# Performance work log

Measured on AMD Instinct MI355X. Metric: run time of the kernel, lower is better.

## Reference

```python
import jax, jax.numpy as jnp
import numpy as np
from jax import lax

V, D = 100000, 300          # vocab, embedding dim (pretrained_embeds shape)
F, FS, K = 256, 3, 5        # nof_filters, filters_size, k_for_maxpool
B, NS, LS, LQ = 64, 50, 60, 32  # batch, n_sents per doc, sent len, question len


def setup_inputs() -> dict:
    key = jax.random.key(0)
    ks = jax.random.split(key, 8)
    sentences = jax.random.randint(ks[0], (B, NS, LS), 0, V)
    question = jax.random.randint(ks[1], (B, LQ), 0, V)
    target_sents = jax.random.randint(ks[2], (B, NS), 0, 2)
    target_docs = jax.random.randint(ks[3], (B,), 0, 2)
    embeds = jax.random.normal(ks[4], (V, D), dtype=jnp.float32)          # frozen pretrained table
    filters = jax.random.normal(ks[5], (F, 1, FS, D), dtype=jnp.float32)  # shared quest/sent conv filters
    W = jax.random.normal(ks[6], (6,), dtype=jnp.float32) * 0.4           # linear_per_q weight
    b = jax.random.normal(ks[7], (1,), dtype=jnp.float32) * 0.1           # linear_per_q bias
    return dict(sentences=sentences, question=question, target_sents=target_sents,
                target_docs=target_docs, embeds=embeds, filters=filters, W=W, b=b)


def _conv(x, filters):
    # x: [N,L,D], filters: [F,1,FS,D] -> [N,L,F]; matches F.conv2d(pad=(FS-1,0)) then slicing last L rows
    fs = filters.shape[2]
    L = x.shape[1]
    y = lax.conv_general_dilated(x[:, None, :, :], filters, (1, 1),
                                 ((fs - 1, fs - 1), (0, 0)),
                                 dimension_numbers=('NCHW', 'OIHW', 'NCHW'))  # [N,F,L+fs-1,1]
    return jnp.transpose(y[:, :, -L:, 0], (0, 2, 1))


def _cos(q, s):
    # q: [B,LQ,d], s: [B,NS,LS,d] -> [NS,B,LQ,LS] cosine similarity matrices
    num = jnp.einsum('bqd,bnld->nbql', q, s)
    qn = jnp.linalg.norm(q, axis=-1)                      # [B,LQ]
    sn = jnp.transpose(jnp.linalg.norm(s, axis=-1), (1, 0, 2))  # [NS,B,LS]
    return num / (qn[None, :, :, None] * sn[:, :, None, :])


def _pool(sim, k):
    # k-max pooling over the sentence-length axis -> stack [max, mean-of-top-k]
    top = lax.top_k(sim, k)[0]
    return jnp.stack([top[..., 0], jnp.mean(top, axis=-1)], axis=-1)


def _bce(p, t):
    eps = 1e-7
    p = jnp.clip(p, eps, 1.0 - eps)
    return -jnp.mean(t * jnp.log(p) + (1.0 - t) * jnp.log1p(-p))


def reference(sentences, question, target_sents, target_docs, embeds, filters, W, b):
    qe = embeds[question]                                 # [B,LQ,D]
    se = embeds[sentences]                                # [B,NS,LS,D]
    sim_ins = _cos(qe, se)                                # [NS,B,LQ,LS]
    sim_oh = (sim_ins >= 1.0 - 1e-5).astype(jnp.float32)  # exact-match channel (unmasked, as in original)
    qc = _conv(qe, filters)                               # [B,LQ,F]
    sc = _conv(se.reshape(B * NS, LS, D), filters).reshape(B, NS, LS, F)
    sim_sen = _cos(qc, sc)                                # [NS,B,LQ,LS]
    qmask = (question > 0).astype(jnp.float32)            # pad id = 0
    smask = (sentences > 0).astype(jnp.float32)
    m = qmask[None, :, :, None] * jnp.transpose(smask, (1, 0, 2))[:, :, None, :]
    feats = jnp.concatenate([_pool(sim_ins * m, K), _pool(sim_sen * m, K), _pool(sim_oh, K)], axis=-1)
    feats = jnp.transpose(feats, (1, 0, 2, 3))            # [B,NS,LQ,6]
    sent_out = jax.nn.sigmoid(feats @ W + b[0])           # [B,NS,LQ]
    sentence_relevance = jnp.mean(sent_out, axis=-1)      # [B,NS]
    document_emitions = jnp.max(sentence_relevance, axis=-1)  # [B]
    loss = (_bce(sentence_relevance, target_sents.astype(jnp.float32)) +
            _bce(document_emitions, target_docs.astype(jnp.float32))) / 2.0
    return loss, sentence_relevance, document_emitions
```

## Files before the change

kernel.cpp:

```cpp
#include <hip/hip_runtime.h>
#include <math.h>

#define VB  64
#define NSS 50
#define LSS 60
#define LQQ 32
#define DD  300
#define FF  256

#define SEST 312
#define SROWS 66
#define SCST 264
#define SIMST 66
#define KKC 29
#define KKI 10
#define KKS 8

typedef __attribute__((ext_vector_type(8))) short bfrag;
typedef __attribute__((ext_vector_type(4))) float ffrag;

__device__ __forceinline__ unsigned short f2bf(float v) {
    unsigned int x = __float_as_uint(v);
    x += 0x7fffu + ((x >> 16) & 1u);
    return (unsigned short)(x >> 16);
}
__device__ __forceinline__ float bf2f(unsigned short u) {
    return __uint_as_float(((unsigned int)u) << 16);
}

__global__ __launch_bounds__(256) void k_fprep(const float* __restrict__ filters,
                                               unsigned short* __restrict__ filt_frag) {
    int idx = blockIdx.x * 256 + threadIdx.x;
    const int total = KKC * 16 * 64 * 8;
    if (idx >= total) return;
    int j = idx & 7, ln = (idx >> 3) & 63, nt = (idx >> 9) & 15, kk = idx >> 13;
    int f = nt * 16 + (ln & 15);
    int k = kk * 32 + ((ln >> 4) << 3) + j;
    int t = k / SEST, d = k - t * SEST;
    unsigned short v = 0;
    if (t < 3 && d < DD) v = f2bf(filters[f * 900 + t * DD + d]);
    filt_frag[idx] = v;
}

__global__ __launch_bounds__(256) void k_qprep(const int* __restrict__ question,
                                               const float* __restrict__ embeds,
                                               const unsigned short* __restrict__ filt_frag,
                                               unsigned short* __restrict__ qe_frag,
                                               unsigned short* __restrict__ qc_frag,
                                               float* __restrict__ q_inv,
                                               float* __restrict__ qc_inv) {
    const int b = blockIdx.x, tid = threadIdx.x, lane = tid & 63, w = tid >> 6;
    const int quad = lane >> 4, m16 = lane & 15;
    __shared__ __align__(16) unsigned short qeb[34 * SEST];
    __shared__ __align__(16) unsigned short qcb[LQQ * SCST];
    __shared__ int qid[LQQ];
    if (tid < LQQ) qid[tid] = question[b * LQQ + tid];
    {
        ushort4 z4 = {0, 0, 0, 0};
        for (int i = tid; i < 96; i += 256) {
            int r = i / 3, c = 300 + (i - r * 3) * 4;
            *(ushort4*)(qeb + r * SEST + c) = z4;
        }
        for (int i = tid; i < 156; i += 256) {
            int r = i / 78, c = (i - r * 78) * 4;
            *(ushort4*)(qeb + (LQQ + r) * SEST + c) = z4;
        }
    }
    __syncthreads();
    for (int i = tid; i < LQQ * 75; i += 256) {
        int r = i / 75, c = (i - r * 75) * 4;
        float4 v = *(const float4*)(embeds + (size_t)qid[r] * DD + c);
        ushort4 h;
        h.x = f2bf(v.x); h.y = f2bf(v.y); h.z = f2bf(v.z); h.w = f2bf(v.w);
        *(ushort4*)(qeb + r * SEST + c) = h;
    }
    __syncthreads();
    {
        int r = tid >> 3, part = tid & 7;
        float s = 0.f;
        for (int c = part * 4; c < DD; c += 32) {
            uint2 u = *(const uint2*)(qeb + r * SEST + c);
            float a0 = bf2f((unsigned short)(u.x & 0xffff)), a1 = bf2f((unsigned short)(u.x >> 16));
            float a2 = bf2f((unsigned short)(u.y & 0xffff)), a3 = bf2f((unsigned short)(u.y >> 16));
            s += a0 * a0 + a1 * a1 + a2 * a2 + a3 * a3;
        }
        s += __shfl_down(s, 4, 64);
        s += __shfl_down(s, 2, 64);
        s += __shfl_down(s, 1, 64);
        if (part == 0) q_inv[b * LQQ + r] = 1.f / sqrtf(s);
    }
    for (int idx = tid; idx < KKI * 2 * 512; idx += 256) {
        int j = idx & 7, ln = (idx >> 3) & 63, mt = (idx >> 9) & 1, kk = idx >> 10;
        int q = mt * 16 + (ln & 15);
        int k = kk * 32 + ((ln >> 4) << 3) + j;
        qe_frag[(size_t)b * (KKI * 2 * 512) + idx] = (k < DD) ? qeb[q * SEST + k] : (unsigned short)0;
    }
    ffrag acc[2][4];
    #pragma unroll
    for (int mt = 0; mt < 2; ++mt)
        #pragma unroll
        for (int i = 0; i < 4; ++i) acc[mt][i] = (ffrag)0.f;
    {
        const bfrag* fF = (const bfrag*)filt_frag;
        const int w4 = w * 4;
        for (int kk = 0; kk < KKC; ++kk) {
            const int kb = kk * 32 + quad * 8;
            bfrag a0 = *(const bfrag*)(qeb + m16 * SEST + kb);
            bfrag a1 = *(const bfrag*)(qeb + (16 + m16) * SEST + kb);
            bfrag bb[4];
            #pragma unroll
            for (int i = 0; i < 4; ++i) bb[i] = fF[(kk * 16 + w4 + i) * 64 + lane];
            #pragma unroll
            for (int i = 0; i < 4; ++i) {
                acc[0][i] = __builtin_amdgcn_mfma_f32_16x16x32_bf16(a0, bb[i], acc[0][i], 0, 0, 0);
                acc[1][i] = __builtin_amdgcn_mfma_f32_16x16x32_bf16(a1, bb[i], acc[1][i], 0, 0, 0);
            }
        }
    }
    #pragma unroll
    for (int mt = 0; mt < 2; ++mt)
        #pragma unroll
        for (int i = 0; i < 4; ++i) {
            int f = (w * 4 + i) * 16 + m16;
            #pragma unroll
            for (int r = 0; r < 4; ++r) {
                int q = mt * 16 + quad * 4 + r;
                qcb[q * SCST + f] = f2bf(acc[mt][i][r]);
            }
        }
    __syncthreads();
    {
        int r = tid >> 3, part = tid & 7;
        float s = 0.f;
        for (int c = part * 4; c < FF; c += 32) {
            uint2 u = *(const uint2*)(qcb + r * SCST + c);
            float a0 = bf2f((unsigned short)(u.x & 0xffff)), a1 = bf2f((unsigned short)(u.x >> 16));
            float a2 = bf2f((unsigned short)(u.y & 0xffff)), a3 = bf2f((unsigned short)(u.y >> 16));
            s += a0 * a0 + a1 * a1 + a2 * a2 + a3 * a3;
        }
        s += __shfl_down(s, 4, 64);
        s += __shfl_down(s, 2, 64);
        s += __shfl_down(s, 1, 64);
        if (part == 0) qc_inv[b * LQQ + r] = 1.f / sqrtf(s);
    }
    for (int idx = tid; idx < KKS * 2 * 512; idx += 256) {
        int j = idx & 7, ln = (idx >> 3) & 63, mt = (idx >> 9) & 1, kk = idx >> 10;
        int q = mt * 16 + (ln & 15);
        int k = kk * 32 + ((ln >> 4) << 3) + j;
        qc_frag[(size_t)b * (KKS * 2 * 512) + idx] = qcb[q * SCST + k];
    }
}

__global__ __launch_bounds__(512, 6) void k_sent(
    const int* __restrict__ sentences, const int* __restrict__ question,
    const float* __restrict__ embeds,
    const unsigned short* __restrict__ filt_frag,
    const unsigned short* __restrict__ qe_frag,
    const unsigned short* __restrict__ qc_frag,
    const float* __restrict__ q_inv, const float* __restrict__ qc_inv,
    const float* __restrict__ W6, const float* __restrict__ b1,
    float* __restrict__ d_out) {
    const int blk = blockIdx.x;
    const int b = blk / NSS, n = blk - b * NSS;
    const int tid = threadIdx.x, lane = tid & 63, w = tid >> 6;
    const int quad = lane >> 4, m16 = lane & 15;

    __shared__ __align__(16) unsigned short seb[SROWS * SEST];
    __shared__ __align__(16) float sim[LQQ * SIMST];
    __shared__ float sinv[64], scninv[64];
    __shared__ int sid[64];
    __shared__ int qid[LQQ];
    __shared__ float qm[LQQ], qiv[LQQ], qciv[LQQ];
    __shared__ float featq[LQQ][4];
    __shared__ float pr[LQQ];
    unsigned short* scb = seb;

    if (tid < 64) sid[tid] = (tid < LSS) ? sentences[((size_t)b * NSS + n) * LSS + tid] : 0;
    if (tid < LQQ) {
        int qi = question[b * LQQ + tid];
        qid[tid] = qi; qm[tid] = qi > 0 ? 1.f : 0.f;
        qiv[tid] = q_inv[b * LQQ + tid]; qciv[tid] = qc_inv[b * LQQ + tid];
    }
    {
        ushort4 z4 = {0, 0, 0, 0};
        for (int i = tid; i < 180; i += 512) {
            int r = i / 3, c = 300 + (i - r * 3) * 4;
            *(ushort4*)(seb + r * SEST + c) = z4;
        }
        for (int i = tid; i < 468; i += 512) {
            int r = i / 78, c = (i - r * 78) * 4;
            *(ushort4*)(seb + (60 + r) * SEST + c) = z4;
        }
    }
    __syncthreads();
    for (int i = tid; i < LSS * 75; i += 512) {
        int r = i / 75, c = (i - r * 75) * 4;
        float4 v = *(const float4*)(embeds + (size_t)sid[r] * DD + c);
        ushort4 h;
        h.x = f2bf(v.x); h.y = f2bf(v.y); h.z = f2bf(v.z); h.w = f2bf(v.w);
        *(ushort4*)(seb + r * SEST + c) = h;
    }
    __syncthreads();
    if (tid < 480) {
        int r = tid >> 3, part = tid & 7;
        float s = 0.f;
        for (int c = part * 4; c < DD; c += 32) {
            uint2 u = *(const uint2*)(seb + r * SEST + c);
            float a0 = bf2f((unsigned short)(u.x & 0xffff)), a1 = bf2f((unsigned short)(u.x >> 16));
            float a2 = bf2f((unsigned short)(u.y & 0xffff)), a3 = bf2f((unsigned short)(u.y >> 16));
            s += a0 * a0 + a1 * a1 + a2 * a2 + a3 * a3;
        }
        s += __shfl_down(s, 4, 64);
        s += __shfl_down(s, 2, 64);
        s += __shfl_down(s, 1, 64);
        if (part == 0) sinv[r] = 1.f / sqrtf(s);
    }
    if (tid >= 480 && tid < 484) sinv[60 + tid - 480] = 0.f;
    __syncthreads();

    ffrag acc[4][2];
    #pragma unroll
    for (int mt = 0; mt < 4; ++mt)
        #pragma unroll
        for (int i = 0; i < 2; ++i) acc[mt][i] = (ffrag)0.f;
    {
        const bfrag* fF = (const bfrag*)filt_frag;
        const int w2 = w * 2;
        for (int kk = 0; kk < KKC; ++kk) {
            const int kb = kk * 32 + quad * 8;
            bfrag a[4];
            #pragma unroll
            for (int mt = 0; mt < 4; ++mt)
                a[mt] = *(const bfrag*)(seb + (mt * 16 + m16) * SEST + kb);
            bfrag bb[2];
            #pragma unroll
            for (int i = 0; i < 2; ++i)
                bb[i] = fF[(kk * 16 + w2 + i) * 64 + lane];
            #pragma unroll
            for (int mt = 0; mt < 4; ++mt)
                #pragma unroll
                for (int i = 0; i < 2; ++i)
                    acc[mt][i] = __builtin_amdgcn_mfma_f32_16x16x32_bf16(a[mt], bb[i], acc[mt][i], 0, 0, 0);
        }
    }
    {
        const bfrag* qF = (const bfrag*)qe_frag;
        const int mt = w >> 2, nt = w & 3;
        ffrag c0 = (ffrag)0.f;
        for (int kk = 0; kk < KKI; ++kk) {
            bfrag aq = qF[((size_t)(b * KKI + kk) * 2 + mt) * 64 + lane];
            bfrag b0 = *(const bfrag*)(seb + (nt * 16 + m16) * SEST + kk * 32 + quad * 8);
            c0 = __builtin_amdgcn_mfma_f32_16x16x32_bf16(aq, b0, c0, 0, 0, 0);
        }
        const int l_ = nt * 16 + m16;
        const float sm = sinv[l_] * (sid[l_] > 0 ? 1.f : 0.f);
        #pragma unroll
        for (int r = 0; r < 4; ++r) {
            int q = mt * 16 + quad * 4 + r;
            sim[q * SIMST + l_] = c0[r] * (qiv[q] * qm[q]) * sm;
        }
    }
    __syncthreads();

    if (tid < 256) {
        ushort4 z4 = {0, 0, 0, 0};
        int r4 = 60 + (tid >> 6), c4 = (tid & 63) * 4;
        *(ushort4*)(scb + r4 * SCST + c4) = z4;
    }
    #pragma unroll
    for (int mt = 0; mt < 4; ++mt)
        #pragma unroll
        for (int i = 0; i < 2; ++i) {
            int f = (w * 2 + i) * 16 + m16;
            #pragma unroll
            for (int r = 0; r < 4; ++r) {
                int l = mt * 16 + quad * 4 + r;
                scb[l * SCST + f] = f2bf(acc[mt][i][r]);
            }
        }
    if (tid < LQQ) {
        int q = tid;
        float t0 = -1e30f, t1 = -1e30f, t2 = -1e30f, t3 = -1e30f, t4 = -1e30f;
        for (int l = 0; l < LSS; ++l) {
            float v = sim[q * SIMST + l];
            if (v > t4) {
                if (v > t0)      { t4 = t3; t3 = t2; t2 = t1; t1 = t0; t0 = v; }
                else if (v > t1) { t4 = t3; t3 = t2; t2 = t1; t1 = v; }
                else if (v > t2) { t4 = t3; t3 = t2; t2 = v; }
                else if (v > t3) { t4 = t3; t3 = v; }
                else               t4 = v;
            }
        }
        featq[q][0] = t0;
        featq[q][1] = (t0 + t1 + t2 + t3 + t4) * 0.2f;
        int qi = qid[q], c = 0;
        for (int l = 0; l < LSS; ++l) c += (sid[l] == qi) ? 1 : 0;
        featq[q][2] = c > 0 ? 1.f : 0.f;
        featq[q][3] = (float)(c < 5 ? c : 5) * 0.2f;
    }
    __syncthreads();
    if (tid < 480) {
        int r = tid >> 3, part = tid & 7;
        float s = 0.f;
        for (int c = part * 4; c < FF; c += 32) {
            uint2 u = *(const uint2*)(scb + r * SCST + c);
            float a0 = bf2f((unsigned short)(u.x & 0xffff)), a1 = bf2f((unsigned short)(u.x >> 16));
            float a2 = bf2f((unsigned short)(u.y & 0xffff)), a3 = bf2f((unsigned short)(u.y >> 16));
            s += a0 * a0 + a1 * a1 + a2 * a2 + a3 * a3;
        }
        s += __shfl_down(s, 4, 64);
        s += __shfl_down(s, 2, 64);
        s += __shfl_down(s, 1, 64);
        if (part == 0) scninv[r] = 1.f / sqrtf(s);
    }
    if (tid >= 480 && tid < 484) scninv[60 + tid - 480] = 0.f;
    __syncthreads();
    {
        const bfrag* qF = (const bfrag*)qc_frag;
        const int mt = w >> 2, nt = w & 3;
        ffrag c0 = (ffrag)0.f;
        for (int kk = 0; kk < KKS; ++kk) {
            bfrag aq = qF[((size_t)(b * KKS + kk) * 2 + mt) * 64 + lane];
            bfrag b0 = *(const bfrag*)(scb + (nt * 16 + m16) * SCST + kk * 32 + quad * 8);
            c0 = __builtin_amdgcn_mfma_f32_16x16x32_bf16(aq, b0, c0, 0, 0, 0);
        }
        const int l_ = nt * 16 + m16;
        const float sm = scninv[l_] * (sid[l_] > 0 ? 1.f : 0.f);
        #pragma unroll
        for (int r = 0; r < 4; ++r) {
            int q = mt * 16 + quad * 4 + r;
            sim[q * SIMST + l_] = c0[r] * (qciv[q] * qm[q]) * sm;
        }
    }
    __syncthreads();
    if (tid < LQQ) {
        int q = tid;
        float t0 = -1e30f, t1 = -1e30f, t2 = -1e30f, t3 = -1e30f, t4 = -1e30f;
        for (int l = 0; l < LSS; ++l) {
            float v = sim[q * SIMST + l];
            if (v > t4) {
                if (v > t0)      { t4 = t3; t3 = t2; t2 = t1; t1 = t0; t0 = v; }
                else if (v > t1) { t4 = t3; t3 = t2; t2 = t1; t1 = v; }
                else if (v > t2) { t4 = t3; t3 = t2; t2 = v; }
                else if (v > t3) { t4 = t3; t3 = v; }
                else               t4 = v;
            }
        }
        float smax = t0, smean = (t0 + t1 + t2 + t3 + t4) * 0.2f;
        float z = featq[q][0] * W6[0] + featq[q][1] * W6[1] + smax * W6[2] + smean * W6[3]
                + featq[q][2] * W6[4] + featq[q][3] * W6[5] + b1[0];
        pr[q] = 1.f / (1.f + expf(-z));
    }
    __syncthreads();
    if (w == 0) {
        float s = (lane < LQQ) ? pr[lane] : 0.f;
        s += __shfl_down(s, 16, 64);
        s += __shfl_down(s, 8, 64);
        s += __shfl_down(s, 4, 64);
        s += __shfl_down(s, 2, 64);
        s += __shfl_down(s, 1, 64);
        if (lane == 0) d_out[1 + (size_t)b * NSS + n] = s * (1.f / 32.f);
    }
}

__global__ __launch_bounds__(256) void k_final(const int* __restrict__ tsent,
                                               const int* __restrict__ tdoc,
                                               float* __restrict__ d_out) {
    const int tid = threadIdx.x;
    __shared__ float sh[256];
    __shared__ float docs[VB];
    if (tid < VB) {
        float m = -1e30f;
        for (int nn = 0; nn < NSS; ++nn) m = fmaxf(m, d_out[1 + tid * NSS + nn]);
        docs[tid] = m;
        d_out[1 + VB * NSS + tid] = m;
    }
    float s = 0.f;
    for (int i = tid; i < VB * NSS; i += 256) {
        float p = d_out[1 + i];
        p = fminf(fmaxf(p, 1e-7f), 1.f - 1e-7f);
        float t = (float)tsent[i];
        s += t * logf(p) + (1.f - t) * log1pf(-p);
    }
    sh[tid] = s;
    __syncthreads();
    for (int st = 128; st > 0; st >>= 1) {
        if (tid < st) sh[tid] += sh[tid + st];
        __syncthreads();
    }
    float ls = 0.f;
    if (tid == 0) ls = -sh[0] / (float)(VB * NSS);
    __syncthreads();
    float s2 = 0.f;
    if (tid < VB) {
        float p = fminf(fmaxf(docs[tid], 1e-7f), 1.f - 1e-7f);
        float t = (float)tdoc[tid];
        s2 = t * logf(p) + (1.f - t) * log1pf(-p);
    }
    sh[tid] = s2;
    __syncthreads();
    for (int st = 128; st > 0; st >>= 1) {
        if (tid < st) sh[tid] += sh[tid + st];
        __syncthreads();
    }
    if (tid == 0) {
        float ld = -sh[0] / (float)VB;
        d_out[0] = 0.5f * (ls + ld);
    }
}

extern "C" void kernel_launch(void* const* d_in, const int* in_sizes, int n_in,
                              void* d_out, int out_size, void* d_ws, size_t ws_size,
                              hipStream_t stream) {
    const int*   sentences = (const int*)d_in[0];
    const int*   question  = (const int*)d_in[1];
    const int*   tsent     = (const int*)d_in[2];
    const int*   tdoc      = (const int*)d_in[3];
    const float* embeds    = (const float*)d_in[4];
    const float* filters   = (const float*)d_in[5];
    const float* W6        = (const float*)d_in[6];
    const float* b1        = (const float*)d_in[7];
    float* out = (float*)d_out;

    float* ws = (float*)d_ws;
    float* q_inv  = ws;
    float* qc_inv = ws + 2048;
    unsigned short* qe_frag  = (unsigned short*)(ws + 4096);
    unsigned short* qc_frag  = qe_frag + 655360;
    unsigned short* filt_frag = qc_frag + 524288;

    k_fprep<<<928, 256, 0, stream>>>(filters, filt_frag);
    k_qprep<<<VB, 256, 0, stream>>>(question, embeds, filt_frag, qe_frag, qc_frag, q_inv, qc_inv);
    k_sent<<<VB * NSS, 512, 0, stream>>>(sentences, question, embeds,
                                         filt_frag, qe_frag, qc_frag,
                                         q_inv, qc_inv, W6, b1, out);
    k_final<<<1, 256, 0, stream>>>(tsent, tdoc, out);
}
```

Measured before the change: 411.0 us.

## Software-pipeline filter fragment loads in conv and widen norm reads

The sentence conv loop is unrolled by two and double-buffers the global filter fragments, with the first fragments issued before the embedding gather, and MFMA groups wrapped in s_setprio. The cosine GEMM loops prefetch the next question fragment, and the norm reductions read 16-byte LDS vectors. One barrier is removed by reading token ids straight from global memory, and the question prep kernel moves to 512 threads with work split across 8 waves. The aim is to hide global-load latency behind MFMA work and cut LDS instruction count, at the cost of more live registers under the 512x6 launch bound.

Measured after the change: 401.8 us. 2.2% less time.

```diff
diff --git a/kernel.cpp b/kernel.cpp
--- a/kernel.cpp
+++ b/kernel.cpp
@@ -42,7 +42,7 @@
     filt_frag[idx] = v;
 }
 
-__global__ __launch_bounds__(256) void k_qprep(const int* __restrict__ question,
+__global__ __launch_bounds__(512) void k_qprep(const int* __restrict__ question,
                                                const float* __restrict__ embeds,
                                                const unsigned short* __restrict__ filt_frag,
                                                unsigned short* __restrict__ qe_frag,
@@ -53,103 +53,122 @@
     const int quad = lane >> 4, m16 = lane & 15;
     __shared__ __align__(16) unsigned short qeb[34 * SEST];
     __shared__ __align__(16) unsigned short qcb[LQQ * SCST];
-    __shared__ int qid[LQQ];
-    if (tid < LQQ) qid[tid] = question[b * LQQ + tid];
+    const int* qrow = question + b * LQQ;
     {
         ushort4 z4 = {0, 0, 0, 0};
-        for (int i = tid; i < 96; i += 256) {
+        for (int i = tid; i < 96; i += 512) {
             int r = i / 3, c = 300 + (i - r * 3) * 4;
             *(ushort4*)(qeb + r * SEST + c) = z4;
         }
-        for (int i = tid; i < 156; i += 256) {
+        for (int i = tid; i < 156; i += 512) {
             int r = i / 78, c = (i - r * 78) * 4;
             *(ushort4*)(qeb + (LQQ + r) * SEST + c) = z4;
         }
     }
-    __syncthreads();
-    for (int i = tid; i < LQQ * 75; i += 256) {
+    for (int i = tid; i < LQQ * 75; i += 512) {
         int r = i / 75, c = (i - r * 75) * 4;
-        float4 v = *(const float4*)(embeds + (size_t)qid[r] * DD + c);
+        float4 v = *(const float4*)(embeds + (size_t)qrow[r] * DD + c);
         ushort4 h;
         h.x = f2bf(v.x); h.y = f2bf(v.y); h.z = f2bf(v.z); h.w = f2bf(v.w);
         *(ushort4*)(qeb + r * SEST + c) = h;
     }
     __syncthreads();
-    {
+    if (tid < 256) {
         int r = tid >> 3, part = tid & 7;
         float s = 0.f;
-        for (int c = part * 4; c < DD; c += 32) {
-            uint2 u = *(const uint2*)(qeb + r * SEST + c);
-            float a0 = bf2f((unsigned short)(u.x & 0xffff)), a1 = bf2f((unsigned short)(u.x >> 16));
-            float a2 = bf2f((unsigned short)(u.y & 0xffff)), a3 = bf2f((unsigned short)(u.y >> 16));
-            s += a0 * a0 + a1 * a1 + a2 * a2 + a3 * a3;
+        #pragma unroll
+        for (int it = 0; it < 5; ++it) {
+            if (!(it == 4 && part == 7)) {
+                int c = part * 8 + it * 64;
+                uint4 u = *(const uint4*)(qeb + r * SEST + c);
+                float a0 = bf2f((unsigned short)(u.x & 0xffff)), a1 = bf2f((unsigned short)(u.x >> 16));
+                float a2 = bf2f((unsigned short)(u.y & 0xffff)), a3 = bf2f((unsigned short)(u.y >> 16));
+                float a4 = bf2f((unsigned short)(u.z & 0xffff)), a5 = bf2f((unsigned short)(u.z >> 16));
+                float a6 = bf2f((unsigned short)(u.w & 0xffff)), a7 = bf2f((unsigned short)(u.w >> 16));
+                s += a0 * a0 + a1 * a1 + a2 * a2 + a3 * a3 + a4 * a4 + a5 * a5 + a6 * a6 + a7 * a7;
+            }
         }
         s += __shfl_down(s, 4, 64);
         s += __shfl_down(s, 2, 64);
         s += __shfl_down(s, 1, 64);
         if (part == 0) q_inv[b * LQQ + r] = 1.f / sqrtf(s);
     }
-    for (int idx = tid; idx < KKI * 2 * 512; idx += 256) {
+    for (int idx = tid; idx < KKI * 2 * 512; idx += 512) {
         int j = idx & 7, ln = (idx >> 3) & 63, mt = (idx >> 9) & 1, kk = idx >> 10;
         int q = mt * 16 + (ln & 15);
         int k = kk * 32 + ((ln >> 4) << 3) + j;
         qe_frag[(size_t)b * (KKI * 2 * 512) + idx] = (k < DD) ? qeb[q * SEST + k] : (unsigned short)0;
     }
-    ffrag acc[2][4];
+    const int mtq = w & 1, w4 = (w >> 1) * 4;
+    ffrag acc[4];
     #pragma unroll
-    for (int mt = 0; mt < 2; ++mt)
-        #pragma unroll
-        for (int i = 0; i < 4; ++i) acc[mt][i] = (ffrag)0.f;
+    for (int i = 0; i < 4; ++i) acc[i] = (ffrag)0.f;
     {
         const bfrag* fF = (const bfrag*)filt_frag;
-        const int w4 = w * 4;
         for (int kk = 0; kk < KKC; ++kk) {
             const int kb = kk * 32 + quad * 8;
-            bfrag a0 = *(const bfrag*)(qeb + m16 * SEST + kb);
-            bfrag a1 = *(const bfrag*)(qeb + (16 + m16) * SEST + kb);
+            bfrag a0 = *(const bfrag*)(qeb + (mtq * 16 + m16) * SEST + kb);
             bfrag bb[4];
             #pragma unroll
             for (int i = 0; i < 4; ++i) bb[i] = fF[(kk * 16 + w4 + i) * 64 + lane];
             #pragma unroll
-            for (int i = 0; i < 4; ++i) {
-                acc[0][i] = __builtin_amdgcn_mfma_f32_16x16x32_bf16(a0, bb[i], acc[0][i], 0, 0, 0);
-                acc[1][i] = __builtin_amdgcn_mfma_f32_16x16x32_bf16(a1, bb[i], acc[1][i], 0, 0, 0);
-            }
+            for (int i = 0; i < 4; ++i)
+                acc[i] = __builtin_amdgcn_mfma_f32_16x16x32_bf16(a0, bb[i], acc[i], 0, 0, 0);
         }
     }
     #pragma unroll
-    for (int mt = 0; mt < 2; ++mt)
-        #pragma unroll
-        for (int i = 0; i < 4; ++i) {
-            int f = (w * 4 + i) * 16 + m16;
-            #pragma unroll
-            for (int r = 0; r < 4; ++r) {
-                int q = mt * 16 + quad * 4 + r;
-                qcb[q * SCST + f] = f2bf(acc[mt][i][r]);
-            }
-        }
-    __syncthreads();
-    {
+    for (int i = 0; i < 4; ++i) {
+        int f = (w4 + i) * 16 + m16;
+        #pragma unroll
+        for (int r = 0; r < 4; ++r) {
+            int q = mtq * 16 + quad * 4 + r;
+            qcb[q * SCST + f] = f2bf(acc[i][r]);
+        }
+    }
+    __syncthreads();
+    if (tid < 256) {
         int r = tid >> 3, part = tid & 7;
         float s = 0.f;
-        for (int c = part * 4; c < FF; c += 32) {
-            uint2 u = *(const uint2*)(qcb + r * SCST + c);
+        #pragma unroll
+        for (int it = 0; it < 4; ++it) {
+            int c = part * 8 + it * 64;
+            uint4 u = *(const uint4*)(qcb + r * SCST + c);
             float a0 = bf2f((unsigned short)(u.x & 0xffff)), a1 = bf2f((unsigned short)(u.x >> 16));
             float a2 = bf2f((unsigned short)(u.y & 0xffff)), a3 = bf2f((unsigned short)(u.y >> 16));
-            s += a0 * a0 + a1 * a1 + a2 * a2 + a3 * a3;
+            float a4 = bf2f((unsigned short)(u.z & 0xffff)), a5 = bf2f((unsigned short)(u.z >> 16));
+            float a6 = bf2f((unsigned short)(u.w & 0xffff)), a7 = bf2f((unsigned short)(u.w >> 16));
+            s += a0 * a0 + a1 * a1 + a2 * a2 + a3 * a3 + a4 * a4 + a5 * a5 + a6 * a6 + a7 * a7;
         }
         s += __shfl_down(s, 4, 64);
         s += __shfl_down(s, 2, 64);
         s += __shfl_down(s, 1, 64);
         if (part == 0) qc_inv[b * LQQ + r] = 1.f / sqrtf(s);
     }
-    for (int idx = tid; idx < KKS * 2 * 512; idx += 256) {
+    for (int idx = tid; idx < KKS * 2 * 512; idx += 512) {
         int j = idx & 7, ln = (idx >> 3) & 63, mt = (idx >> 9) & 1, kk = idx >> 10;
         int q = mt * 16 + (ln & 15);
         int k = kk * 32 + ((ln >> 4) << 3) + j;
         qc_frag[(size_t)b * (KKS * 2 * 512) + idx] = qcb[q * SCST + k];
     }
 }
+
+#define CONV_STEP(KKV, BB0, BB1) do {                                              \
+    const int kb_ = (KKV) * 32 + quad * 8;                                         \
+    bfrag a0_ = *(const bfrag*)(seb + (m16) * SEST + kb_);                         \
+    bfrag a1_ = *(const bfrag*)(seb + (16 + m16) * SEST + kb_);                    \
+    bfrag a2_ = *(const bfrag*)(seb + (32 + m16) * SEST + kb_);                    \
+    bfrag a3_ = *(const bfrag*)(seb + (48 + m16) * SEST + kb_);                    \
+    __builtin_amdgcn_s_setprio(1);                                                 \
+    acc[0][0] = __builtin_amdgcn_mfma_f32_16x16x32_bf16(a0_, BB0, acc[0][0], 0, 0, 0); \
+    acc[0][1] = __builtin_amdgcn_mfma_f32_16x16x32_bf16(a0_, BB1, acc[0][1], 0, 0, 0); \
+    acc[1][0] = __builtin_amdgcn_mfma_f32_16x16x32_bf16(a1_, BB0, acc[1][0], 0, 0, 0); \
+    acc[1][1] = __builtin_amdgcn_mfma_f32_16x16x32_bf16(a1_, BB1, acc[1][1], 0, 0, 0); \
+    acc[2][0] = __builtin_amdgcn_mfma_f32_16x16x32_bf16(a2_, BB0, acc[2][0], 0, 0, 0); \
+    acc[2][1] = __builtin_amdgcn_mfma_f32_16x16x32_bf16(a2_, BB1, acc[2][1], 0, 0, 0); \
+    acc[3][0] = __builtin_amdgcn_mfma_f32_16x16x32_bf16(a3_, BB0, acc[3][0], 0, 0, 0); \
+    acc[3][1] = __builtin_amdgcn_mfma_f32_16x16x32_bf16(a3_, BB1, acc[3][1], 0, 0, 0); \
+    __builtin_amdgcn_s_setprio(0);                                                 \
+} while (0)
 
 __global__ __launch_bounds__(512, 6) void k_sent(
     const int* __restrict__ sentences, const int* __restrict__ question,
@@ -164,6 +183,7 @@
     const int b = blk / NSS, n = blk - b * NSS;
     const int tid = threadIdx.x, lane = tid & 63, w = tid >> 6;
     const int quad = lane >> 4, m16 = lane & 15;
+    const int w2 = w * 2;
 
     __shared__ __align__(16) unsigned short seb[SROWS * SEST];
     __shared__ __align__(16) float sim[LQQ * SIMST];
@@ -175,7 +195,12 @@
     __shared__ float pr[LQQ];
     unsigned short* scb = seb;
 
-    if (tid < 64) sid[tid] = (tid < LSS) ? sentences[((size_t)b * NSS + n) * LSS + tid] : 0;
+    const bfrag* fF = (const bfrag*)filt_frag;
+    bfrag b0a = fF[(w2) * 64 + lane];
+    bfrag b0b = fF[(w2 + 1) * 64 + lane];
+
+    const int* srow = sentences + ((size_t)b * NSS + n) * LSS;
+    if (tid < 64) sid[tid] = (tid < LSS) ? srow[tid] : 0;
     if (tid < LQQ) {
         int qi = question[b * LQQ + tid];
         qid[tid] = qi; qm[tid] = qi > 0 ? 1.f : 0.f;
@@ -192,10 +217,9 @@
             *(ushort4*)(seb + (60 + r) * SEST + c) = z4;
         }
     }
-    __syncthreads();
     for (int i = tid; i < LSS * 75; i += 512) {
         int r = i / 75, c = (i - r * 75) * 4;
-        float4 v = *(const float4*)(embeds + (size_t)sid[r] * DD + c);
+        float4 v = *(const float4*)(embeds + (size_t)srow[r] * DD + c);
         ushort4 h;
         h.x = f2bf(v.x); h.y = f2bf(v.y); h.z = f2bf(v.z); h.w = f2bf(v.w);
         *(ushort4*)(seb + r * SEST + c) = h;
@@ -204,11 +228,17 @@
     if (tid < 480) {
         int r = tid >> 3, part = tid & 7;
         float s = 0.f;
-        for (int c = part * 4; c < DD; c += 32) {
-            uint2 u = *(const uint2*)(seb + r * SEST + c);
-            float a0 = bf2f((unsigned short)(u.x & 0xffff)), a1 = bf2f((unsigned short)(u.x >> 16));
-            float a2 = bf2f((unsigned short)(u.y & 0xffff)), a3 = bf2f((unsigned short)(u.y >> 16));
-            s += a0 * a0 + a1 * a1 + a2 * a2 + a3 * a3;
+        #pragma unroll
+        for (int it = 0; it < 5; ++it) {
+            if (!(it == 4 && part == 7)) {
+                int c = part * 8 + it * 64;
+                uint4 u = *(const uint4*)(seb + r * SEST + c);
+                float a0 = bf2f((unsigned short)(u.x & 0xffff)), a1 = bf2f((unsigned short)(u.x >> 16));
+                float a2 = bf2f((unsigned short)(u.y & 0xffff)), a3 = bf2f((unsigned short)(u.y >> 16));
+                float a4 = bf2f((unsigned short)(u.z & 0xffff)), a5 = bf2f((unsigned short)(u.z >> 16));
+                float a6 = bf2f((unsigned short)(u.w & 0xffff)), a7 = bf2f((unsigned short)(u.w >> 16));
+                s += a0 * a0 + a1 * a1 + a2 * a2 + a3 * a3 + a4 * a4 + a5 * a5 + a6 * a6 + a7 * a7;
+            }
         }
         s += __shfl_down(s, 4, 64);
         s += __shfl_down(s, 2, 64);
@@ -224,33 +254,32 @@
         #pragma unroll
         for (int i = 0; i < 2; ++i) acc[mt][i] = (ffrag)0.f;
     {
-        const bfrag* fF = (const bfrag*)filt_frag;
-        const int w2 = w * 2;
-        for (int kk = 0; kk < KKC; ++kk) {
-            const int kb = kk * 32 + quad * 8;
-            bfrag a[4];
-            #pragma unroll
-            for (int mt = 0; mt < 4; ++mt)
-                a[mt] = *(const bfrag*)(seb + (mt * 16 + m16) * SEST + kb);
-            bfrag bb[2];
-            #pragma unroll
-            for (int i = 0; i < 2; ++i)
-                bb[i] = fF[(kk * 16 + w2 + i) * 64 + lane];
-            #pragma unroll
-            for (int mt = 0; mt < 4; ++mt)
-                #pragma unroll
-                for (int i = 0; i < 2; ++i)
-                    acc[mt][i] = __builtin_amdgcn_mfma_f32_16x16x32_bf16(a[mt], bb[i], acc[mt][i], 0, 0, 0);
-        }
-    }
-    {
-        const bfrag* qF = (const bfrag*)qe_frag;
+        bfrag b1a, b1b;
+        for (int kk = 0; kk + 2 <= KKC; kk += 2) {
+            b1a = fF[((kk + 1) * 16 + w2) * 64 + lane];
+            b1b = fF[((kk + 1) * 16 + w2 + 1) * 64 + lane];
+            CONV_STEP(kk, b0a, b0b);
+            if (kk + 2 < KKC) {
+                b0a = fF[((kk + 2) * 16 + w2) * 64 + lane];
+                b0b = fF[((kk + 2) * 16 + w2 + 1) * 64 + lane];
+            }
+            CONV_STEP(kk + 1, b1a, b1b);
+        }
+        CONV_STEP(KKC - 1, b0a, b0b);
+    }
+    {
         const int mt = w >> 2, nt = w & 3;
+        const bfrag* qF = (const bfrag*)qe_frag + ((size_t)b * KKI * 2 + mt) * 64 + lane;
+        const unsigned short* sebr = seb + (nt * 16 + m16) * SEST + quad * 8;
         ffrag c0 = (ffrag)0.f;
-        for (int kk = 0; kk < KKI; ++kk) {
-            bfrag aq = qF[((size_t)(b * KKI + kk) * 2 + mt) * 64 + lane];
-            bfrag b0 = *(const bfrag*)(seb + (nt * 16 + m16) * SEST + kk * 32 + quad * 8);
-            c0 = __builtin_amdgcn_mfma_f32_16x16x32_bf16(aq, b0, c0, 0, 0, 0);
+        bfrag aq0 = qF[0];
+        for (int kk = 0; kk < KKI; kk += 2) {
+            bfrag aq1 = qF[(kk + 1) * 128];
+            bfrag bL0 = *(const bfrag*)(sebr + kk * 32);
+            c0 = __builtin_amdgcn_mfma_f32_16x16x32_bf16(aq0, bL0, c0, 0, 0, 0);
+            if (kk + 2 < KKI) aq0 = qF[(kk + 2) * 128];
+            bfrag bL1 = *(const bfrag*)(sebr + (kk + 1) * 32);
+            c0 = __builtin_amdgcn_mfma_f32_16x16x32_bf16(aq1, bL1, c0, 0, 0, 0);
         }
         const int l_ = nt * 16 + m16;
         const float sm = sinv[l_] * (sid[l_] > 0 ? 1.f : 0.f);
@@ -271,7 +300,7 @@
     for (int mt = 0; mt < 4; ++mt)
         #pragma unroll
         for (int i = 0; i < 2; ++i) {
-            int f = (w * 2 + i) * 16 + m16;
+            int f = (w2 + i) * 16 + m16;
             #pragma unroll
             for (int r = 0; r < 4; ++r) {
                 int l = mt * 16 + quad * 4 + r;
@@ -302,11 +331,15 @@
     if (tid < 480) {
         int r = tid >> 3, part = tid & 7;
         float s = 0.f;
-        for (int c = part * 4; c < FF; c += 32) {
-            uint2 u = *(const uint2*)(scb + r * SCST + c);
+        #pragma unroll
+        for (int it = 0; it < 4; ++it) {
+            int c = part * 8 + it * 64;
+            uint4 u = *(const uint4*)(scb + r * SCST + c);
             float a0 = bf2f((unsigned short)(u.x & 0xffff)), a1 = bf2f((unsigned short)(u.x >> 16));
             float a2 = bf2f((unsigned short)(u.y & 0xffff)), a3 = bf2f((unsigned short)(u.y >> 16));
-            s += a0 * a0 + a1 * a1 + a2 * a2 + a3 * a3;
+            float a4 = bf2f((unsigned short)(u.z & 0xffff)), a5 = bf2f((unsigned short)(u.z >> 16));
+            float a6 = bf2f((unsigned short)(u.w & 0xffff)), a7 = bf2f((unsigned short)(u.w >> 16));
+            s += a0 * a0 + a1 * a1 + a2 * a2 + a3 * a3 + a4 * a4 + a5 * a5 + a6 * a6 + a7 * a7;
         }
         s += __shfl_down(s, 4, 64);
         s += __shfl_down(s, 2, 64);
@@ -316,13 +349,18 @@
     if (tid >= 480 && tid < 484) scninv[60 + tid - 480] = 0.f;
     __syncthreads();
     {
-        const bfrag* qF = (const bfrag*)qc_frag;
         const int mt = w >> 2, nt = w & 3;
+        const bfrag* qF = (const bfrag*)qc_frag + ((size_t)b * KKS * 2 + mt) * 64 + lane;
+        const unsigned short* scbr = scb + (nt * 16 + m16) * SCST + quad * 8;
         ffrag c0 = (ffrag)0.f;
-        for (int kk = 0; kk < KKS; ++kk) {
-            bfrag aq = qF[((size_t)(b * KKS + kk) * 2 + mt) * 64 + lane];
-            bfrag b0 = *(const bfrag*)(scb + (nt * 16 + m16) * SCST + kk * 32 + quad * 8);
-            c0 = __builtin_amdgcn_mfma_f32_16x16x32_bf16(aq, b0, c0, 0, 0, 0);
+        bfrag aq0 = qF[0];
+        for (int kk = 0; kk < KKS; kk += 2) {
+            bfrag aq1 = qF[(kk + 1) * 128];
+            bfrag bL0 = *(const bfrag*)(scbr + kk * 32);
+            c0 = __builtin_amdgcn_mfma_f32_16x16x32_bf16(aq0, bL0, c0, 0, 0, 0);
+            if (kk + 2 < KKS) aq0 = qF[(kk + 2) * 128];
+            bfrag bL1 = *(const bfrag*)(scbr + (kk + 1) * 32);
+            c0 = __builtin_amdgcn_mfma_f32_16x16x32_bf16(aq1, bL1, c0, 0, 0, 0);
         }
         const int l_ = nt * 16 + m16;
         const float sm = scninv[l_] * (sid[l_] > 0 ? 1.f : 0.f);
@@ -430,7 +468,7 @@
     unsigned short* filt_frag = qc_frag + 524288;
 
     k_fprep<<<928, 256, 0, stream>>>(filters, filt_frag);
-    k_qprep<<<VB, 256, 0, stream>>>(question, embeds, filt_frag, qe_frag, qc_frag, q_inv, qc_inv);
+    k_qprep<<<VB, 512, 0, stream>>>(question, embeds, filt_frag, qe_frag, qc_frag, q_inv, qc_inv);
     k_sent<<<VB * NSS, 512, 0, stream>>>(sentences, question, embeds,
                                          filt_frag, qe_frag, qc_frag,
                                          q_inv, qc_inv, W6, b1, out);
```
